# Optimization experiments

Measured on AMD Instinct MI355X. Metric: run time of the kernel, lower is better.

The kernel has to match this reference:

```python
import jax, jax.numpy as jnp
import numpy as np

B, M, N, E = 64, 100, 6400, 102400   # graphs, nodes/graph, total nodes, edges
H, D, EMB, IMG, NC = 4, 512, 768, 1024, 2
HD = H * D
EPS = 1e-5


def _bn2(x, g, b, m, v):
    # BatchNorm1d eval mode on [B, C]
    return (x - m) / jnp.sqrt(v + EPS) * g + b


def _bn3(x, g, b, m, v):
    # BatchNorm1d eval mode on [B, C, L] -> channel dim is axis 1 (node index)
    return (x - m[None, :, None]) / jnp.sqrt(v + EPS)[None, :, None] * g[None, :, None] + b[None, :, None]


def _gat(feat, src, dst, W, al, ar, bias):
    # DGL GATConv (eval: feat_drop is identity). feat: [N, F_in]
    h = (feat @ W.T).reshape(-1, H, D)                 # [N, H, D]
    el = (h * al[None]).sum(-1)                         # [N, H]
    er = (h * ar[None]).sum(-1)                         # [N, H]
    e = jax.nn.leaky_relu(el[src] + er[dst], negative_slope=0.2)  # [E, H]
    mx = jax.ops.segment_max(e, dst, num_segments=N)
    a = jnp.exp(e - mx[dst])
    s = jax.ops.segment_sum(a, dst, num_segments=N)
    alpha = a / s[dst]                                  # edge softmax over incoming edges
    out = jax.ops.segment_sum(h[src] * alpha[:, :, None], dst, num_segments=N)  # [N, H, D]
    return out + bias.reshape(1, H, D)


def setup_inputs() -> dict:
    key = jax.random.key(0)
    ks = iter(jax.random.split(key, 80))
    n = lambda *s: jax.random.normal(next(ks), s, dtype=jnp.float32)

    def bn(c):
        return (1.0 + 0.1 * n(c), 0.1 * n(c), 0.1 * n(c),
                0.5 + jax.random.uniform(next(ks), (c,), dtype=jnp.float32))

    s = 0.02
    inp = {}
    inp['img_embedding'] = n(B, IMG)
    inp['func_text_embedding'] = n(B, EMB)
    inp['unix_emb'] = n(N, EMB)
    inp['pos_emb'] = jax.random.uniform(next(ks), (N, 4), dtype=jnp.float32)
    inp['src'] = jax.random.randint(next(ks), (E,), 0, N)
    inp['dst'] = jax.random.randint(next(ks), (E,), 0, N)
    inp['gat1_W'] = n(HD, EMB) * s; inp['gat1_al'] = n(H, D) * 0.1; inp['gat1_ar'] = n(H, D) * 0.1; inp['gat1_b'] = jnp.zeros(HD)
    inp['gat2_W'] = n(HD, HD) * s; inp['gat2_al'] = n(H, D) * 0.1; inp['gat2_ar'] = n(H, D) * 0.1; inp['gat2_b'] = jnp.zeros(HD)
    inp['fc_W'] = n(D, HD) * s; inp['fc_b'] = jnp.zeros(D)
    inp['hidden_W'] = n(8, D, D) * s; inp['hidden_b'] = jnp.zeros((8, D))
    inp['bn_text_g'], inp['bn_text_b'], inp['bn_text_m'], inp['bn_text_v'] = bn(EMB)
    inp['fc_text_W'] = n(D, EMB) * s; inp['fc_text_b'] = jnp.zeros(D)
    inp['swin_g'], inp['swin_b'], inp['swin_m'], inp['swin_v'] = bn(IMG)
    inp['swinfc_W'] = n(D, IMG) * s; inp['swinfc_b'] = jnp.zeros(D)
    inp['bngat_g'], inp['bngat_b'], inp['bngat_m'], inp['bngat_v'] = bn(M)
    inp['fc_gat_W'] = n(480, D) * s; inp['fc_gat_b'] = jnp.zeros(480)
    inp['bnbb_g'], inp['bnbb_b'], inp['bnbb_m'], inp['bnbb_v'] = bn(M)
    inp['fc_bbox_W'] = n(32, 4) * s; inp['fc_bbox_b'] = jnp.zeros(32)
    inp['fbn_g'], inp['fbn_b'], inp['fbn_m'], inp['fbn_v'] = bn(3 * D)
    inp['final_W'] = n(NC, 3 * D) * s; inp['final_b'] = jnp.zeros(NC)
    return inp


def reference(img_embedding, func_text_embedding, unix_emb, pos_emb, src, dst,
              gat1_W, gat1_al, gat1_ar, gat1_b, gat2_W, gat2_al, gat2_ar, gat2_b,
              fc_W, fc_b, hidden_W, hidden_b,
              bn_text_g, bn_text_b, bn_text_m, bn_text_v, fc_text_W, fc_text_b,
              swin_g, swin_b, swin_m, swin_v, swinfc_W, swinfc_b,
              bngat_g, bngat_b, bngat_m, bngat_v, fc_gat_W, fc_gat_b,
              bnbb_g, bnbb_b, bnbb_m, bnbb_v, fc_bbox_W, fc_bbox_b,
              fbn_g, fbn_b, fbn_m, fbn_v, final_W, final_b):
    # image branch
    x = jax.nn.elu(_bn2(img_embedding, swin_g, swin_b, swin_m, swin_v) @ swinfc_W.T + swinfc_b)
    # text branch
    ft = jax.nn.elu(_bn2(func_text_embedding, bn_text_g, bn_text_b, bn_text_m, bn_text_v) @ fc_text_W.T + fc_text_b)
    # graph branch: two stacked GATConv layers (dropout is identity in eval)
    h = _gat(unix_emb, src, dst, gat1_W, gat1_al, gat1_ar, gat1_b).reshape(N, HD)
    h = _gat(h, src, dst, gat2_W, gat2_al, gat2_ar, gat2_b).reshape(N, HD)
    h = jax.nn.elu(h @ fc_W.T + fc_b)
    for i in range(8):
        h = jax.nn.elu(h @ hidden_W[i].T + hidden_b[i])
    # unbatch + pad to max_node=100 -> pure reshape (all graphs have exactly M nodes)
    h_i = h.reshape(B, M, D)
    pos_i = pos_emb.reshape(B, M, 4)
    h_i = jax.nn.elu(_bn3(h_i, bngat_g, bngat_b, bngat_m, bngat_v) @ fc_gat_W.T + fc_gat_b)      # [B, M, 480]
    pos_i = jax.nn.elu(_bn3(pos_i, bnbb_g, bnbb_b, bnbb_m, bnbb_v) @ fc_bbox_W.T + fc_bbox_b)    # [B, M, 32]
    h_feature = jnp.concatenate([h_i, pos_i], axis=2).mean(axis=1)                                # [B, 512]
    all_feats = jnp.concatenate([x, h_feature, ft], axis=1)                                       # [B, 1536]
    return _bn2(all_feats, fbn_g, fbn_b, fbn_m, fbn_v) @ final_W.T + final_b
```

## Files before the change

### kernel.cpp

```cpp
#include <hip/hip_runtime.h>
#include <math.h>

#define Bg   64
#define Mg   100
#define Ng   6400
#define Eg   102400
#define Hh   4
#define Dd   512
#define HDd  2048
#define EMBd 768
#define IMGd 1024
#define EPSc 1e-5f

typedef __bf16 bf16x8 __attribute__((ext_vector_type(8)));
typedef float  f32x4  __attribute__((ext_vector_type(4)));

#define SBAR __builtin_amdgcn_sched_barrier(0)
#define WBAR __builtin_amdgcn_s_barrier()

__device__ __forceinline__ float eluf(float x) { return x > 0.f ? x : expm1f(x); }

__device__ __forceinline__ unsigned short f2bf(float x) {
    unsigned int u = __builtin_bit_cast(unsigned int, x);
    u += 0x7FFFu + ((u >> 16) & 1u);
    return (unsigned short)(u >> 16);
}
__device__ __forceinline__ float bf2f(unsigned short s) {
    return __builtin_bit_cast(float, ((unsigned int)s) << 16);
}

__device__ __forceinline__ void gld16(const void* g, void* l) {
    __builtin_amdgcn_global_load_lds(
        (const __attribute__((address_space(1))) void*)g,
        (__attribute__((address_space(3))) void*)l, 16, 0, 0);
}

__global__ __launch_bounds__(256)
void gemm_bf16(const unsigned short* __restrict__ A,
               const unsigned short* __restrict__ W,
               const float* __restrict__ bias, void* __restrict__ C,
               int M, int N, int K, int act, int outbf)
{
    __shared__ __align__(16) unsigned short As[2][128 * 32];
    __shared__ __align__(16) unsigned short Bs[2][128 * 32];
    const int tid  = threadIdx.x;
    const int lane = tid & 63, wid = tid >> 6;
    const int bm = blockIdx.y * 128, bn = blockIdx.x * 128;
    const int wm = (wid >> 1) * 64, wn = (wid & 1) * 64;
    const int lrow = lane >> 2;
    const int lcol = (lane & 3) << 3;

    f32x4 acc[4][4] = {};

    const int ra = wid * 32;
    const unsigned short* gA0 = A + (size_t)(bm + ra + lrow) * K + lcol;
    const unsigned short* gA1 = A + (size_t)(bm + ra + 16 + lrow) * K + lcol;
    int rb0 = bn + ra + lrow;       if (rb0 >= N) rb0 = N - 1;
    int rb1 = bn + ra + 16 + lrow;  if (rb1 >= N) rb1 = N - 1;
    const unsigned short* gB0 = W + (size_t)rb0 * K + lcol;
    const unsigned short* gB1 = W + (size_t)rb1 * K + lcol;

    const int frow = lane & 15;
    const int quad = (lane >> 4) << 3;
    const int nt = K >> 5;

#define STAGE128(t, b)                                  \
    do {                                                \
        const int k0_ = (t) << 5;                       \
        gld16(gA0 + k0_, &As[b][ra * 32]);              \
        gld16(gA1 + k0_, &As[b][(ra + 16) * 32]);       \
        gld16(gB0 + k0_, &Bs[b][ra * 32]);              \
        gld16(gB1 + k0_, &Bs[b][(ra + 16) * 32]);       \
    } while (0)

    STAGE128(0, 0);
    if (nt > 1) STAGE128(1, 1);

    for (int t = 0; t < nt; ++t) {
        const int bi = t & 1;
        SBAR;
        if (t + 1 < nt) { asm volatile("s_waitcnt vmcnt(4)" ::: "memory"); }
        else            { asm volatile("s_waitcnt vmcnt(0)" ::: "memory"); }
        SBAR; WBAR; SBAR;

        bf16x8 af[4], bfr[4];
#pragma unroll
        for (int i = 0; i < 4; ++i)
            af[i]  = *(const bf16x8*)&As[bi][(wm + i * 16 + frow) * 32 + quad];
#pragma unroll
        for (int i = 0; i < 4; ++i)
            bfr[i] = *(const bf16x8*)&Bs[bi][(wn + i * 16 + frow) * 32 + quad];
#pragma unroll
        for (int mi = 0; mi < 4; ++mi)
#pragma unroll
            for (int ni = 0; ni < 4; ++ni)
                acc[mi][ni] = __builtin_amdgcn_mfma_f32_16x16x32_bf16(
                    af[mi], bfr[ni], acc[mi][ni], 0, 0, 0);

        SBAR;
        asm volatile("s_waitcnt lgkmcnt(0)" ::: "memory");
        SBAR; WBAR; SBAR;
        if (t + 2 < nt) STAGE128(t + 2, bi);
    }
#undef STAGE128

    const int crow0 = bm + wm + ((lane >> 4) << 2);
    const int ccol0 = bn + wn + (lane & 15);
#pragma unroll
    for (int mi = 0; mi < 4; ++mi) {
#pragma unroll
        for (int ni = 0; ni < 4; ++ni) {
            int col = ccol0 + ni * 16;
            if (col >= N) continue;
            float bv = bias ? bias[col] : 0.f;
#pragma unroll
            for (int r = 0; r < 4; ++r) {
                int row = crow0 + mi * 16 + r;
                float v = acc[mi][ni][r] + bv;
                if (act) v = eluf(v);
                if (outbf) ((unsigned short*)C)[(size_t)row * N + col] = f2bf(v);
                else       ((float*)C)[(size_t)row * N + col] = v;
            }
        }
    }
}

__global__ __launch_bounds__(256)
void gemm_bf16_t64(const unsigned short* __restrict__ A,
                   const unsigned short* __restrict__ W,
                   const float* __restrict__ bias, void* __restrict__ C,
                   int M, int N, int K, int act, int outbf)
{
    __shared__ __align__(16) unsigned short As[2][64 * 32];
    __shared__ __align__(16) unsigned short Bs[2][64 * 32];
    const int tid  = threadIdx.x;
    const int lane = tid & 63, wid = tid >> 6;
    const int bm = blockIdx.y * 64, bn = blockIdx.x * 64;
    const int wm = (wid >> 1) * 32, wn = (wid & 1) * 32;
    const int lrow = lane >> 2;
    const int lcol = (lane & 3) << 3;

    f32x4 acc[2][2] = {};

    const int ra = wid * 16;
    const unsigned short* gA = A + (size_t)(bm + ra + lrow) * K + lcol;
    int rb = bn + ra + lrow; if (rb >= N) rb = N - 1;
    const unsigned short* gB = W + (size_t)rb * K + lcol;

    const int frow = lane & 15;
    const int quad = (lane >> 4) << 3;
    const int nt = K >> 5;

#define STAGE64(t, b)                           \
    do {                                        \
        const int k0_ = (t) << 5;               \
        gld16(gA + k0_, &As[b][ra * 32]);       \
        gld16(gB + k0_, &Bs[b][ra * 32]);       \
    } while (0)

    STAGE64(0, 0);
    if (nt > 1) STAGE64(1, 1);

    for (int t = 0; t < nt; ++t) {
        const int bi = t & 1;
        SBAR;
        if (t + 1 < nt) { asm volatile("s_waitcnt vmcnt(2)" ::: "memory"); }
        else            { asm volatile("s_waitcnt vmcnt(0)" ::: "memory"); }
        SBAR; WBAR; SBAR;

        bf16x8 af0 = *(const bf16x8*)&As[bi][(wm + frow) * 32 + quad];
        bf16x8 af1 = *(const bf16x8*)&As[bi][(wm + 16 + frow) * 32 + quad];
        bf16x8 bf0 = *(const bf16x8*)&Bs[bi][(wn + frow) * 32 + quad];
        bf16x8 bf1 = *(const bf16x8*)&Bs[bi][(wn + 16 + frow) * 32 + quad];
        acc[0][0] = __builtin_amdgcn_mfma_f32_16x16x32_bf16(af0, bf0, acc[0][0], 0, 0, 0);
        acc[0][1] = __builtin_amdgcn_mfma_f32_16x16x32_bf16(af0, bf1, acc[0][1], 0, 0, 0);
        acc[1][0] = __builtin_amdgcn_mfma_f32_16x16x32_bf16(af1, bf0, acc[1][0], 0, 0, 0);
        acc[1][1] = __builtin_amdgcn_mfma_f32_16x16x32_bf16(af1, bf1, acc[1][1], 0, 0, 0);

        SBAR;
        asm volatile("s_waitcnt lgkmcnt(0)" ::: "memory");
        SBAR; WBAR; SBAR;
        if (t + 2 < nt) STAGE64(t + 2, bi);
    }
#undef STAGE64

    const int crow0 = bm + wm + ((lane >> 4) << 2);
    const int ccol0 = bn + wn + (lane & 15);
#pragma unroll
    for (int mi = 0; mi < 2; ++mi) {
#pragma unroll
        for (int ni = 0; ni < 2; ++ni) {
            int col = ccol0 + ni * 16;
            if (col >= N) continue;
            float bv = bias ? bias[col] : 0.f;
#pragma unroll
            for (int r = 0; r < 4; ++r) {
                int row = crow0 + mi * 16 + r;
                float v = acc[mi][ni][r] + bv;
                if (act) v = eluf(v);
                if (outbf) ((unsigned short*)C)[(size_t)row * N + col] = f2bf(v);
                else       ((float*)C)[(size_t)row * N + col] = v;
            }
        }
    }
}

__global__ __launch_bounds__(256)
void gemm_nt(const float* __restrict__ A, const float* __restrict__ W,
             const float* __restrict__ bias, float* __restrict__ C,
             int M, int N, int K, int act)
{
    __shared__ float As[16 * 68];
    __shared__ float Ws[16 * 68];
    const int tid = threadIdx.x;
    const int tx = tid & 15, ty = tid >> 4;
    const int bm = blockIdx.y * 64, bn = blockIdx.x * 64;
    const int lrow = tid >> 2;
    const int lk4  = (tid & 3) << 2;
    const int arow = bm + lrow;
    const int wrow = bn + lrow;
    const float* Aptr = A + (size_t)arow * K + lk4;
    const float* Wptr = W + (size_t)wrow * K + lk4;
    float acc[4][4] = {{0.f,0.f,0.f,0.f},{0.f,0.f,0.f,0.f},{0.f,0.f,0.f,0.f},{0.f,0.f,0.f,0.f}};

    for (int k0 = 0; k0 < K; k0 += 16) {
        float4 av = make_float4(0.f,0.f,0.f,0.f);
        float4 wv = make_float4(0.f,0.f,0.f,0.f);
        if (arow < M) av = *(const float4*)(Aptr + k0);
        if (wrow < N) wv = *(const float4*)(Wptr + k0);
        As[(lk4+0)*68 + lrow] = av.x;
        As[(lk4+1)*68 + lrow] = av.y;
        As[(lk4+2)*68 + lrow] = av.z;
        As[(lk4+3)*68 + lrow] = av.w;
        Ws[(lk4+0)*68 + lrow] = wv.x;
        Ws[(lk4+1)*68 + lrow] = wv.y;
        Ws[(lk4+2)*68 + lrow] = wv.z;
        Ws[(lk4+3)*68 + lrow] = wv.w;
        __syncthreads();
#pragma unroll
        for (int kk = 0; kk < 16; ++kk) {
            float4 a = *(const float4*)&As[kk*68 + (ty<<2)];
            float4 w = *(const float4*)&Ws[kk*68 + (tx<<2)];
            acc[0][0] += a.x*w.x; acc[0][1] += a.x*w.y; acc[0][2] += a.x*w.z; acc[0][3] += a.x*w.w;
            acc[1][0] += a.y*w.x; acc[1][1] += a.y*w.y; acc[1][2] += a.y*w.z; acc[1][3] += a.y*w.w;
            acc[2][0] += a.z*w.x; acc[2][1] += a.z*w.y; acc[2][2] += a.z*w.z; acc[2][3] += a.z*w.w;
            acc[3][0] += a.w*w.x; acc[3][1] += a.w*w.y; acc[3][2] += a.w*w.z; acc[3][3] += a.w*w.w;
        }
        __syncthreads();
    }

#pragma unroll
    for (int i = 0; i < 4; ++i) {
        int row = bm + (ty<<2) + i;
        int col = bn + (tx<<2);
        if (row < M && col < N) {
            float4 v;
            v.x = acc[i][0]; v.y = acc[i][1]; v.z = acc[i][2]; v.w = acc[i][3];
            if (bias) { v.x += bias[col]; v.y += bias[col+1]; v.z += bias[col+2]; v.w += bias[col+3]; }
            if (act == 1) { v.x = eluf(v.x); v.y = eluf(v.y); v.z = eluf(v.z); v.w = eluf(v.w); }
            *(float4*)(C + (size_t)row * N + col) = v;
        }
    }
}

struct CvtPack {
    const float* s[6];
    unsigned short* d[6];
    int n4[6];
};

__global__ void cvt_all(CvtPack p, int total4)
{
    int i = blockIdx.x * 256 + threadIdx.x;
    if (i >= total4) return;
#pragma unroll
    for (int k = 0; k < 6; ++k) {
        if (i < p.n4[k]) {
            float4 v = ((const float4*)p.s[k])[i];
            ushort4 o;
            o.x = f2bf(v.x); o.y = f2bf(v.y); o.z = f2bf(v.z); o.w = f2bf(v.w);
            ((ushort4*)p.d[k])[i] = o;
            return;
        }
        i -= p.n4[k];
    }
}

__global__ void bn_col(const float* __restrict__ x, const float* __restrict__ g,
                       const float* __restrict__ b, const float* __restrict__ m,
                       const float* __restrict__ v, float* __restrict__ y,
                       int rows, int cols)
{
    int i = blockIdx.x * 256 + threadIdx.x;
    if (i >= rows * cols) return;
    int c = i % cols;
    float inv = rsqrtf(v[c] + EPSc);
    y[i] = (x[i] - m[c]) * inv * g[c] + b[c];
}

__global__ void bn_node_b4(const ushort4* __restrict__ x, const float* __restrict__ g,
                           const float* __restrict__ b, const float* __restrict__ m,
                           const float* __restrict__ v, ushort4* __restrict__ y,
                           int total4, int Cdim4)
{
    int i = blockIdx.x * 256 + threadIdx.x;
    if (i >= total4) return;
    int n = i / Cdim4;
    int p = n % Mg;
    float sc = rsqrtf(v[p] + EPSc) * g[p];
    float sh = b[p] - m[p] * sc;
    ushort4 xv = x[i];
    ushort4 o;
    o.x = f2bf(bf2f(xv.x) * sc + sh);
    o.y = f2bf(bf2f(xv.y) * sc + sh);
    o.z = f2bf(bf2f(xv.z) * sc + sh);
    o.w = f2bf(bf2f(xv.w) * sc + sh);
    y[i] = o;
}

__global__ void zero_i32(int* __restrict__ p, int n)
{
    int i = blockIdx.x * 256 + threadIdx.x;
    if (i < n) p[i] = 0;
}

__global__ void count_dst(const int* __restrict__ dst, int* __restrict__ counts, int E)
{
    int i = blockIdx.x * 256 + threadIdx.x;
    if (i < E) atomicAdd(&counts[dst[i]], 1);
}

__global__ __launch_bounds__(1024)
void scan_excl(const int* __restrict__ counts, int* __restrict__ offs,
               int* __restrict__ cursor, int n)
{
    __shared__ int sm[1024];
    __shared__ int carry;
    if (threadIdx.x == 0) carry = 0;
    __syncthreads();
    for (int base = 0; base < n; base += 1024) {
        int i = base + (int)threadIdx.x;
        int v = (i < n) ? counts[i] : 0;
        sm[threadIdx.x] = v;
        __syncthreads();
        for (int o = 1; o < 1024; o <<= 1) {
            int t = (threadIdx.x >= (unsigned)o) ? sm[threadIdx.x - o] : 0;
            __syncthreads();
            sm[threadIdx.x] += t;
            __syncthreads();
        }
        int incl = sm[threadIdx.x];
        int myc = carry;
        if (i < n) {
            int ex = myc + incl - v;
            offs[i] = ex;
            cursor[i] = ex;
        }
        __syncthreads();
        if (threadIdx.x == 1023) carry = myc + sm[1023];
        __syncthreads();
    }
    if (threadIdx.x == 0) offs[n] = carry;
}

__global__ void scatter_edges(const int* __restrict__ dst, int* __restrict__ cursor,
                              int* __restrict__ eid, int E)
{
    int i = blockIdx.x * 256 + threadIdx.x;
    if (i < E) {
        int p = atomicAdd(&cursor[dst[i]], 1);
        eid[p] = i;
    }
}

__global__ __launch_bounds__(256)
void elr_kernel(const unsigned short* __restrict__ Hm, const float* __restrict__ al,
                const float* __restrict__ ar, float* __restrict__ el,
                float* __restrict__ er)
{
    int wid = threadIdx.x >> 6, lane = threadIdx.x & 63;
    int g = (blockIdx.x << 2) + wid;
    int n = g >> 2, h = g & 3;
    const unsigned short* hp = Hm + ((size_t)n << 11) + (h << 9) + (lane << 3);
    const float* alp = al + (h << 9) + (lane << 3);
    const float* arp = ar + (h << 9) + (lane << 3);
    ushort4 x0 = *(const ushort4*)hp;
    ushort4 x1 = *(const ushort4*)(hp + 4);
    float4 l0 = *(const float4*)alp, l1 = *(const float4*)(alp + 4);
    float4 r0 = *(const float4*)arp, r1 = *(const float4*)(arp + 4);
    float a0 = bf2f(x0.x), a1 = bf2f(x0.y), a2 = bf2f(x0.z), a3 = bf2f(x0.w);
    float a4 = bf2f(x1.x), a5 = bf2f(x1.y), a6 = bf2f(x1.z), a7 = bf2f(x1.w);
    float se = a0*l0.x + a1*l0.y + a2*l0.z + a3*l0.w + a4*l1.x + a5*l1.y + a6*l1.z + a7*l1.w;
    float sr = a0*r0.x + a1*r0.y + a2*r0.z + a3*r0.w + a4*r1.x + a5*r1.y + a6*r1.z + a7*r1.w;
#pragma unroll
    for (int o = 32; o > 0; o >>= 1) {
        se += __shfl_down(se, o, 64);
        sr += __shfl_down(sr, o, 64);
    }
    if (lane == 0) { el[g] = se; er[g] = sr; }
}

__global__ __launch_bounds__(256)
void gat_agg(const unsigned short* __restrict__ Hm, const float* __restrict__ el,
             const float* __restrict__ er, const int* __restrict__ src,
             const int* __restrict__ offs, const int* __restrict__ eid,
             const float* __restrict__ bias, unsigned short* __restrict__ out)
{
    int n = blockIdx.x;
    int tid = threadIdx.x;
    int beg = offs[n], end = offs[n + 1];
    int deg = end - beg;
    const int b0 = tid << 2;
    const int b1 = 1024 + (tid << 2);
    const int h0 = tid >> 7;
    const int h1 = h0 + 2;

    if (deg == 0) {
#pragma unroll
        for (int j = 0; j < 4; ++j) {
            out[((size_t)n << 11) + b0 + j] = f2bf(bias[b0 + j]);
            out[((size_t)n << 11) + b1 + j] = f2bf(bias[b1 + j]);
        }
        return;
    }

    __shared__ float m_sh[4], s_sh[4], al_sh[4];
    __shared__ int   src_sh[128];
    __shared__ float logit_sh[512];
    __shared__ float w_sh[512];

    if (tid < 4) { m_sh[tid] = -INFINITY; s_sh[tid] = 0.f; }
    float acc[8] = {0.f,0.f,0.f,0.f,0.f,0.f,0.f,0.f};
    __syncthreads();

    for (int c0 = 0; c0 < deg; c0 += 128) {
        int cnt = min(128, deg - c0);
        for (int i = tid; i < cnt; i += 256) src_sh[i] = src[eid[beg + c0 + i]];
        __syncthreads();
        for (int idx = tid; idx < (cnt << 2); idx += 256) {
            int i = idx >> 2, h = idx & 3;
            float x = el[(src_sh[i] << 2) + h] + er[(n << 2) + h];
            logit_sh[idx] = x > 0.f ? x : 0.2f * x;
        }
        __syncthreads();
        if (tid < 4) {
            float cm = -INFINITY;
            for (int i = 0; i < cnt; ++i) cm = fmaxf(cm, logit_sh[(i << 2) + tid]);
            float mn = fmaxf(m_sh[tid], cm);
            al_sh[tid] = expf(m_sh[tid] - mn);
            m_sh[tid] = mn;
        }
        __syncthreads();
        for (int idx = tid; idx < (cnt << 2); idx += 256)
            w_sh[idx] = expf(logit_sh[idx] - m_sh[idx & 3]);
        __syncthreads();
        if (tid < 4) {
            float cs = 0.f;
            for (int i = 0; i < cnt; ++i) cs += w_sh[(i << 2) + tid];
            s_sh[tid] = s_sh[tid] * al_sh[tid] + cs;
        }
        float r0 = al_sh[h0], r1 = al_sh[h1];
        acc[0] *= r0; acc[1] *= r0; acc[2] *= r0; acc[3] *= r0;
        acc[4] *= r1; acc[5] *= r1; acc[6] *= r1; acc[7] *= r1;
        for (int i = 0; i < cnt; ++i) {
            const unsigned short* hp = Hm + ((size_t)src_sh[i] << 11);
            ushort4 a = *(const ushort4*)(hp + b0);
            ushort4 b = *(const ushort4*)(hp + b1);
            float w0 = w_sh[(i << 2) + h0], w1 = w_sh[(i << 2) + h1];
            acc[0] += w0 * bf2f(a.x); acc[1] += w0 * bf2f(a.y);
            acc[2] += w0 * bf2f(a.z); acc[3] += w0 * bf2f(a.w);
            acc[4] += w1 * bf2f(b.x); acc[5] += w1 * bf2f(b.y);
            acc[6] += w1 * bf2f(b.z); acc[7] += w1 * bf2f(b.w);
        }
        __syncthreads();
    }

    float is0 = 1.f / s_sh[h0], is1 = 1.f / s_sh[h1];
#pragma unroll
    for (int j = 0; j < 4; ++j) {
        out[((size_t)n << 11) + b0 + j] = f2bf(acc[j] * is0 + bias[b0 + j]);
        out[((size_t)n << 11) + b1 + j] = f2bf(acc[4 + j] * is1 + bias[b1 + j]);
    }
}

__global__ void mean_kernel(const float* __restrict__ hg, const float* __restrict__ pos,
                            const float* __restrict__ bg, const float* __restrict__ bb_,
                            const float* __restrict__ bm_, const float* __restrict__ bv_,
                            const float* __restrict__ W, const float* __restrict__ bias,
                            float* __restrict__ hf)
{
    int i = blockIdx.x * 256 + threadIdx.x;
    if (i >= Bg * Dd) return;
    int bb = i >> 9, c = i & 511;
    float s = 0.f;
    if (c < 480) {
        const float* p = hg + (size_t)bb * Mg * 480 + c;
        for (int mm = 0; mm < Mg; ++mm) s += p[mm * 480];
    } else {
        int o = c - 480;
        float w0 = W[(o << 2) + 0], w1 = W[(o << 2) + 1];
        float w2 = W[(o << 2) + 2], w3 = W[(o << 2) + 3];
        float bo = bias[o];
        const float* pp = pos + (size_t)bb * Mg * 4;
        for (int mm = 0; mm < Mg; ++mm) {
            float sc = rsqrtf(bv_[mm] + EPSc) * bg[mm];
            float sh = bb_[mm] - bm_[mm] * sc;
            float a = bo + (pp[mm*4+0]*sc+sh)*w0 + (pp[mm*4+1]*sc+sh)*w1
                         + (pp[mm*4+2]*sc+sh)*w2 + (pp[mm*4+3]*sc+sh)*w3;
            s += eluf(a);
        }
    }
    hf[i] = s * 0.01f;
}

__global__ __launch_bounds__(256)
void final_kernel(const float* __restrict__ x, const float* __restrict__ hf,
                  const float* __restrict__ ft, const float* __restrict__ g,
                  const float* __restrict__ b, const float* __restrict__ m,
                  const float* __restrict__ v, const float* __restrict__ W,
                  const float* __restrict__ bias, float* __restrict__ out)
{
    int bb = blockIdx.x;
    int tid = threadIdx.x;
    float a0 = 0.f, a1 = 0.f;
    for (int c = tid; c < 1536; c += 256) {
        float xv = (c < 512) ? x[bb * 512 + c]
                 : (c < 1024) ? hf[bb * 512 + (c - 512)]
                              : ft[bb * 512 + (c - 1024)];
        float z = (xv - m[c]) * rsqrtf(v[c] + EPSc) * g[c] + b[c];
        a0 += z * W[c];
        a1 += z * W[1536 + c];
    }
    __shared__ float r0[256], r1[256];
    r0[tid] = a0; r1[tid] = a1;
    __syncthreads();
    for (int o = 128; o > 0; o >>= 1) {
        if (tid < o) { r0[tid] += r0[tid + o]; r1[tid] += r1[tid + o]; }
        __syncthreads();
    }
    if (tid == 0) {
        out[bb * 2 + 0] = r0[0] + bias[0];
        out[bb * 2 + 1] = r1[0] + bias[1];
    }
}

extern "C" void kernel_launch(void* const* d_in, const int* in_sizes, int n_in,
                              void* d_out, int out_size, void* d_ws, size_t ws_size,
                              hipStream_t stream)
{
    (void)in_sizes; (void)n_in; (void)out_size; (void)ws_size;

    const float* img   = (const float*)d_in[0];
    const float* ftxt  = (const float*)d_in[1];
    const float* unixe = (const float*)d_in[2];
    const float* pos   = (const float*)d_in[3];
    const int*   src   = (const int*)  d_in[4];
    const int*   dst   = (const int*)  d_in[5];
    const float* g1W   = (const float*)d_in[6];
    const float* g1al  = (const float*)d_in[7];
    const float* g1ar  = (const float*)d_in[8];
    const float* g1b   = (const float*)d_in[9];
    const float* g2W   = (const float*)d_in[10];
    const float* g2al  = (const float*)d_in[11];
    const float* g2ar  = (const float*)d_in[12];
    const float* g2b   = (const float*)d_in[13];
    const float* fcW   = (const float*)d_in[14];
    const float* fcb   = (const float*)d_in[15];
    const float* hidW  = (const float*)d_in[16];
    const float* hidb  = (const float*)d_in[17];
    const float* btg   = (const float*)d_in[18];
    const float* btb   = (const float*)d_in[19];
    const float* btm   = (const float*)d_in[20];
    const float* btv   = (const float*)d_in[21];
    const float* ftW   = (const float*)d_in[22];
    const float* ftbi  = (const float*)d_in[23];
    const float* swg   = (const float*)d_in[24];
    const float* swb   = (const float*)d_in[25];
    const float* swm   = (const float*)d_in[26];
    const float* swv   = (const float*)d_in[27];
    const float* swW   = (const float*)d_in[28];
    const float* swbi  = (const float*)d_in[29];
    const float* bgg   = (const float*)d_in[30];
    const float* bgb   = (const float*)d_in[31];
    const float* bgm   = (const float*)d_in[32];
    const float* bgv   = (const float*)d_in[33];
    const float* fgW   = (const float*)d_in[34];
    const float* fgb   = (const float*)d_in[35];
    const float* bbgp  = (const float*)d_in[36];
    const float* bbbp  = (const float*)d_in[37];
    const float* bbmp  = (const float*)d_in[38];
    const float* bbvp  = (const float*)d_in[39];
    const float* fbW   = (const float*)d_in[40];
    const float* fbb   = (const float*)d_in[41];
    const float* fng   = (const float*)d_in[42];
    const float* fnb   = (const float*)d_in[43];
    const float* fnm   = (const float*)d_in[44];
    const float* fnv   = (const float*)d_in[45];
    const float* fiW   = (const float*)d_in[46];
    const float* fib   = (const float*)d_in[47];
    float* out = (float*)d_out;

    char* p = (char*)d_ws;
    unsigned short* fA  = (unsigned short*)p; p += (size_t)Ng * HDd * 2;
    unsigned short* fB  = (unsigned short*)p; p += (size_t)Ng * HDd * 2;
    unsigned short* fC  = (unsigned short*)p; p += (size_t)Ng * Dd * 2;
    unsigned short* fD  = (unsigned short*)p; p += (size_t)Ng * Dd * 2;
    float*          fE  = (float*)p;          p += (size_t)Ng * 480 * 4;
    float*          el  = (float*)p;          p += (size_t)Ng * Hh * 4;
    float*          er  = (float*)p;          p += (size_t)Ng * Hh * 4;
    float*          xb  = (float*)p;          p += (size_t)Bg * Dd * 4;
    float*          ftb = (float*)p;          p += (size_t)Bg * Dd * 4;
    float*          hf  = (float*)p;          p += (size_t)Bg * Dd * 4;
    float*          ti  = (float*)p;          p += (size_t)Bg * IMGd * 4;
    float*          tt  = (float*)p;          p += (size_t)Bg * EMBd * 4;
    unsigned short* ubf = (unsigned short*)p; p += (size_t)Ng * EMBd * 2;
    unsigned short* wg1 = (unsigned short*)p; p += (size_t)HDd * EMBd * 2;
    unsigned short* wg2 = (unsigned short*)p; p += (size_t)HDd * HDd * 2;
    unsigned short* wfc = (unsigned short*)p; p += (size_t)Dd * HDd * 2;
    unsigned short* whid= (unsigned short*)p; p += (size_t)8 * Dd * Dd * 2;
    unsigned short* wfg = (unsigned short*)p; p += (size_t)480 * Dd * 2;
    int* counts = (int*)p; p += (size_t)Ng * 4;
    int* offs   = (int*)p; p += (size_t)(Ng + 1) * 4 + 12;
    int* cursor = (int*)p; p += (size_t)Ng * 4;
    int* eid    = (int*)p; p += (size_t)Eg * 4;

    CvtPack cp;
    cp.s[0] = unixe; cp.d[0] = ubf;  cp.n4[0] = Ng * EMBd / 4;
    cp.s[1] = g1W;   cp.d[1] = wg1;  cp.n4[1] = HDd * EMBd / 4;
    cp.s[2] = g2W;   cp.d[2] = wg2;  cp.n4[2] = HDd * HDd / 4;
    cp.s[3] = fcW;   cp.d[3] = wfc;  cp.n4[3] = Dd * HDd / 4;
    cp.s[4] = hidW;  cp.d[4] = whid; cp.n4[4] = 8 * Dd * Dd / 4;
    cp.s[5] = fgW;   cp.d[5] = wfg;  cp.n4[5] = 480 * Dd / 4;
    int total4 = cp.n4[0] + cp.n4[1] + cp.n4[2] + cp.n4[3] + cp.n4[4] + cp.n4[5];
    cvt_all<<<(total4 + 255)/256, 256, 0, stream>>>(cp, total4);

    bn_col<<<(Bg*IMGd + 255)/256, 256, 0, stream>>>(img, swg, swb, swm, swv, ti, Bg, IMGd);
    gemm_nt<<<dim3(8, 1), 256, 0, stream>>>(ti, swW, swbi, xb, Bg, Dd, IMGd, 1);
    bn_col<<<(Bg*EMBd + 255)/256, 256, 0, stream>>>(ftxt, btg, btb, btm, btv, tt, Bg, EMBd);
    gemm_nt<<<dim3(8, 1), 256, 0, stream>>>(tt, ftW, ftbi, ftb, Bg, Dd, EMBd, 1);

    zero_i32<<<(Ng + 255)/256, 256, 0, stream>>>(counts, Ng);
    count_dst<<<(Eg + 255)/256, 256, 0, stream>>>(dst, counts, Eg);
    scan_excl<<<1, 1024, 0, stream>>>(counts, offs, cursor, Ng);
    scatter_edges<<<(Eg + 255)/256, 256, 0, stream>>>(dst, cursor, eid, Eg);

    gemm_bf16<<<dim3(HDd/128, Ng/128), 256, 0, stream>>>(ubf, wg1, nullptr, fA, Ng, HDd, EMBd, 0, 1);
    elr_kernel<<<Ng, 256, 0, stream>>>(fA, g1al, g1ar, el, er);
    gat_agg<<<Ng, 256, 0, stream>>>(fA, el, er, src, offs, eid, g1b, fB);

    gemm_bf16<<<dim3(HDd/128, Ng/128), 256, 0, stream>>>(fB, wg2, nullptr, fA, Ng, HDd, HDd, 0, 1);
    elr_kernel<<<Ng, 256, 0, stream>>>(fA, g2al, g2ar, el, er);
    gat_agg<<<Ng, 256, 0, stream>>>(fA, el, er, src, offs, eid, g2b, fB);

    gemm_bf16_t64<<<dim3(Dd/64, Ng/64), 256, 0, stream>>>(fB, wfc, fcb, fC, Ng, Dd, HDd, 1, 1);

    unsigned short* cur = fC; unsigned short* nxt = fD;
    for (int i = 0; i < 8; ++i) {
        gemm_bf16_t64<<<dim3(Dd/64, Ng/64), 256, 0, stream>>>(
            cur, whid + (size_t)i * Dd * Dd, hidb + (size_t)i * Dd, nxt, Ng, Dd, Dd, 1, 1);
        unsigned short* t = cur; cur = nxt; nxt = t;
    }

    bn_node_b4<<<(Ng*Dd/4 + 255)/256, 256, 0, stream>>>(
        (const ushort4*)cur, bgg, bgb, bgm, bgv, (ushort4*)nxt, Ng*Dd/4, Dd/4);
    gemm_bf16_t64<<<dim3(8, Ng/64), 256, 0, stream>>>(nxt, wfg, fgb, fE, Ng, 480, Dd, 1, 0);

    mean_kernel<<<(Bg*Dd + 255)/256, 256, 0, stream>>>(fE, pos, bbgp, bbbp, bbmp, bbvp, fbW, fbb, hf);

    final_kernel<<<Bg, 256, 0, stream>>>(xb, hf, ftb, fng, fnb, fnm, fnv, fiW, fib, out);
}
```

Measured before the change: 818.9 us.

## Replace GAT projection GEMM with 256x256-tile, 8-wave pipelined swizzled kernel

Adds a new bf16 GEMM for the two GAT projections that uses 256x256 output tiles, 512 threads, a K-step of 64, XOR-swizzled LDS layout and a finely interleaved load/MFMA schedule with setprio hints. The aim is more data reuse per block and less LDS bank conflict and stall time. The trade-off is a far smaller grid (200 blocks for 256 CUs), 128 KB of LDS per block, and the loss of the N bounds check.

```diff
diff --git a/kernel.cpp b/kernel.cpp
--- a/kernel.cpp
+++ b/kernel.cpp
@@ -17,6 +17,7 @@
 
 #define SBAR __builtin_amdgcn_sched_barrier(0)
 #define WBAR __builtin_amdgcn_s_barrier()
+#define BARRIER do { SBAR; WBAR; SBAR; } while (0)
 
 __device__ __forceinline__ float eluf(float x) { return x > 0.f ? x : expm1f(x); }
 
@@ -35,88 +36,144 @@
         (__attribute__((address_space(3))) void*)l, 16, 0, 0);
 }
 
-__global__ __launch_bounds__(256)
-void gemm_bf16(const unsigned short* __restrict__ A,
-               const unsigned short* __restrict__ W,
-               const float* __restrict__ bias, void* __restrict__ C,
-               int M, int N, int K, int act, int outbf)
-{
-    __shared__ __align__(16) unsigned short As[2][128 * 32];
-    __shared__ __align__(16) unsigned short Bs[2][128 * 32];
+__global__ __launch_bounds__(512, 2)
+void gemm_bf16_256(const unsigned short* __restrict__ A,
+                   const unsigned short* __restrict__ W,
+                   const float* __restrict__ bias, void* __restrict__ C,
+                   int M, int N, int K, int act, int outbf)
+{
+    __shared__ __align__(16) unsigned short As[2][256 * 64];
+    __shared__ __align__(16) unsigned short Bs[2][256 * 64];
+
     const int tid  = threadIdx.x;
     const int lane = tid & 63, wid = tid >> 6;
-    const int bm = blockIdx.y * 128, bn = blockIdx.x * 128;
-    const int wm = (wid >> 1) * 64, wn = (wid & 1) * 64;
-    const int lrow = lane >> 2;
-    const int lcol = (lane & 3) << 3;
-
-    f32x4 acc[4][4] = {};
-
-    const int ra = wid * 32;
-    const unsigned short* gA0 = A + (size_t)(bm + ra + lrow) * K + lcol;
-    const unsigned short* gA1 = A + (size_t)(bm + ra + 16 + lrow) * K + lcol;
-    int rb0 = bn + ra + lrow;       if (rb0 >= N) rb0 = N - 1;
-    int rb1 = bn + ra + 16 + lrow;  if (rb1 >= N) rb1 = N - 1;
-    const unsigned short* gB0 = W + (size_t)rb0 * K + lcol;
-    const unsigned short* gB1 = W + (size_t)rb1 * K + lcol;
-
-    const int frow = lane & 15;
-    const int quad = (lane >> 4) << 3;
-    const int nt = K >> 5;
-
-#define STAGE128(t, b)                                  \
-    do {                                                \
-        const int k0_ = (t) << 5;                       \
-        gld16(gA0 + k0_, &As[b][ra * 32]);              \
-        gld16(gA1 + k0_, &As[b][(ra + 16) * 32]);       \
-        gld16(gB0 + k0_, &Bs[b][ra * 32]);              \
-        gld16(gB1 + k0_, &Bs[b][(ra + 16) * 32]);       \
+    const int wm = wid >> 2, wn = wid & 3;
+    const int bm = blockIdx.y * 256, bn = blockIdx.x * 256;
+    const int fl = lane & 15;
+    const int kb = (lane >> 4) << 4;
+    const int sx = ((lane >> 2) & 1) << 5;
+
+    f32x4 acc[8][4] = {};
+    bf16x8 a_[4][2];
+    bf16x8 b_[2][2][2];
+
+    const int NT = K >> 6;
+
+    const int srow0 = tid >> 3;
+    const int scol  = (((tid & 7) ^ (((tid >> 5) & 1) << 1)) << 3);
+    const unsigned short* pAs = A + (size_t)(bm + srow0) * K + scol;
+    const unsigned short* pBs = W + (size_t)(bn + srow0) * K + scol;
+    const size_t K64 = (size_t)K * 64, K128 = (size_t)K * 128;
+
+#define STGA(kt, h, d)                                                        \
+    do {                                                                      \
+        gld16(pAs + (h) * K128 + ((kt) << 6),                                 \
+              (char*)As[d] + (h) * 16384 + wid * 1024);                       \
+        gld16(pAs + (h) * K128 + K64 + ((kt) << 6),                           \
+              (char*)As[d] + (h) * 16384 + 8192 + wid * 1024);                \
     } while (0)
-
-    STAGE128(0, 0);
-    if (nt > 1) STAGE128(1, 1);
-
-    for (int t = 0; t < nt; ++t) {
-        const int bi = t & 1;
+#define STGB(kt, h, d)                                                        \
+    do {                                                                      \
+        gld16(pBs + (h) * K128 + ((kt) << 6),                                 \
+              (char*)Bs[d] + (h) * 16384 + wid * 1024);                       \
+        gld16(pBs + (h) * K128 + K64 + ((kt) << 6),                           \
+              (char*)Bs[d] + (h) * 16384 + 8192 + wid * 1024);                \
+    } while (0)
+
+#define LDA(qm, d)                                                            \
+    _Pragma("unroll") for (int i = 0; i < 4; ++i)                             \
+    _Pragma("unroll") for (int kk = 0; kk < 2; ++kk) {                        \
+        int r_  = wm * 128 + (qm) * 64 + i * 16 + fl;                         \
+        int pb_ = r_ * 128 + ((kk * 64 + kb) ^ sx);                           \
+        a_[i][kk] = *(const bf16x8*)((const char*)As[d] + pb_);               \
+    }
+#define LDB(qn, d)                                                            \
+    _Pragma("unroll") for (int j = 0; j < 2; ++j)                             \
+    _Pragma("unroll") for (int kk = 0; kk < 2; ++kk) {                        \
+        int r_  = wn * 64 + (qn) * 32 + j * 16 + fl;                          \
+        int pb_ = r_ * 128 + ((kk * 64 + kb) ^ sx);                           \
+        b_[qn][j][kk] = *(const bf16x8*)((const char*)Bs[d] + pb_);           \
+    }
+#define MM(qm, qn)                                                            \
+    do {                                                                      \
+        __builtin_amdgcn_s_setprio(1);                                        \
+        _Pragma("unroll") for (int kk = 0; kk < 2; ++kk)                      \
+        _Pragma("unroll") for (int i = 0; i < 4; ++i)                         \
+        _Pragma("unroll") for (int j = 0; j < 2; ++j)                         \
+            acc[(qm) * 4 + i][(qn) * 2 + j] =                                 \
+                __builtin_amdgcn_mfma_f32_16x16x32_bf16(                      \
+                    a_[i][kk], b_[qn][j][kk],                                 \
+                    acc[(qm) * 4 + i][(qn) * 2 + j], 0, 0, 0);                \
+        __builtin_amdgcn_s_setprio(0);                                        \
+    } while (0)
+
+    STGB(0, 0, 0); STGB(0, 1, 0);
+    STGA(0, 0, 0); STGA(0, 1, 0);
+    STGB(1, 0, 1); STGB(1, 1, 1);
+    SBAR; asm volatile("s_waitcnt vmcnt(4)" ::: "memory"); SBAR;
+    BARRIER;
+
+    for (int j = 0; j < (NT >> 1); ++j) {
+        const int O = 2 * j + 1;
+        const int g1 = (2 * j + 2 < NT), g2 = (2 * j + 3 < NT);
+
+        LDA(0, 0); LDB(0, 0);
+        STGA(O, 0, 1);
+        BARRIER; MM(0, 0); BARRIER;
+
+        LDB(1, 0);
+        STGA(O, 1, 1);
+        BARRIER; MM(0, 1); BARRIER;
+
+        LDA(1, 0);
+        if (g1) STGB(2 * j + 2, 0, 0);
+        BARRIER; MM(1, 0); BARRIER;
+
+        if (g1) STGB(2 * j + 2, 1, 0);
         SBAR;
-        if (t + 1 < nt) { asm volatile("s_waitcnt vmcnt(4)" ::: "memory"); }
-        else            { asm volatile("s_waitcnt vmcnt(0)" ::: "memory"); }
-        SBAR; WBAR; SBAR;
-
-        bf16x8 af[4], bfr[4];
-#pragma unroll
-        for (int i = 0; i < 4; ++i)
-            af[i]  = *(const bf16x8*)&As[bi][(wm + i * 16 + frow) * 32 + quad];
-#pragma unroll
-        for (int i = 0; i < 4; ++i)
-            bfr[i] = *(const bf16x8*)&Bs[bi][(wn + i * 16 + frow) * 32 + quad];
-#pragma unroll
-        for (int mi = 0; mi < 4; ++mi)
-#pragma unroll
-            for (int ni = 0; ni < 4; ++ni)
-                acc[mi][ni] = __builtin_amdgcn_mfma_f32_16x16x32_bf16(
-                    af[mi], bfr[ni], acc[mi][ni], 0, 0, 0);
-
+        if (g1) { asm volatile("s_waitcnt vmcnt(4)" ::: "memory"); }
+        else    { asm volatile("s_waitcnt vmcnt(0)" ::: "memory"); }
         SBAR;
-        asm volatile("s_waitcnt lgkmcnt(0)" ::: "memory");
-        SBAR; WBAR; SBAR;
-        if (t + 2 < nt) STAGE128(t + 2, bi);
-    }
-#undef STAGE128
-
-    const int crow0 = bm + wm + ((lane >> 4) << 2);
-    const int ccol0 = bn + wn + (lane & 15);
-#pragma unroll
-    for (int mi = 0; mi < 4; ++mi) {
-#pragma unroll
-        for (int ni = 0; ni < 4; ++ni) {
-            int col = ccol0 + ni * 16;
-            if (col >= N) continue;
+        BARRIER; MM(1, 1); BARRIER;
+
+        LDA(0, 1); LDB(0, 1);
+        if (g1) STGA(2 * j + 2, 0, 0);
+        BARRIER; MM(0, 0); BARRIER;
+
+        LDB(1, 1);
+        if (g1) STGA(2 * j + 2, 1, 0);
+        BARRIER; MM(0, 1); BARRIER;
+
+        LDA(1, 1);
+        if (g2) STGB(2 * j + 3, 0, 1);
+        BARRIER; MM(1, 0); BARRIER;
+
+        if (g2) STGB(2 * j + 3, 1, 1);
+        SBAR;
+        if (g1) { asm volatile("s_waitcnt vmcnt(4)" ::: "memory"); }
+        else    { asm volatile("s_waitcnt vmcnt(0)" ::: "memory"); }
+        SBAR;
+        BARRIER; MM(1, 1); BARRIER;
+    }
+
+#undef STGA
+#undef STGB
+#undef LDA
+#undef LDB
+#undef MM
+
+    const int crow0 = bm + wm * 128 + ((lane >> 4) << 2);
+    const int ccol0 = bn + wn * 64 + fl;
+#pragma unroll
+    for (int fr = 0; fr < 8; ++fr) {
+#pragma unroll
+        for (int fc = 0; fc < 4; ++fc) {
+            int col = ccol0 + fc * 16;
             float bv = bias ? bias[col] : 0.f;
 #pragma unroll
-            for (int r = 0; r < 4; ++r) {
-                int row = crow0 + mi * 16 + r;
-                float v = acc[mi][ni][r] + bv;
+            for (int rr = 0; rr < 4; ++rr) {
+                int row = crow0 + fr * 16 + rr;
+                float v = acc[fr][fc][rr] + bv;
                 if (act) v = eluf(v);
                 if (outbf) ((unsigned short*)C)[(size_t)row * N + col] = f2bf(v);
                 else       ((float*)C)[(size_t)row * N + col] = v;
@@ -644,11 +701,11 @@
     scan_excl<<<1, 1024, 0, stream>>>(counts, offs, cursor, Ng);
     scatter_edges<<<(Eg + 255)/256, 256, 0, stream>>>(dst, cursor, eid, Eg);
 
-    gemm_bf16<<<dim3(HDd/128, Ng/128), 256, 0, stream>>>(ubf, wg1, nullptr, fA, Ng, HDd, EMBd, 0, 1);
+    gemm_bf16_256<<<dim3(HDd/256, Ng/256), 512, 0, stream>>>(ubf, wg1, nullptr, fA, Ng, HDd, EMBd, 0, 1);
     elr_kernel<<<Ng, 256, 0, stream>>>(fA, g1al, g1ar, el, er);
     gat_agg<<<Ng, 256, 0, stream>>>(fA, el, er, src, offs, eid, g1b, fB);
 
-    gemm_bf16<<<dim3(HDd/128, Ng/128), 256, 0, stream>>>(fB, wg2, nullptr, fA, Ng, HDd, HDd, 0, 1);
+    gemm_bf16_256<<<dim3(HDd/256, Ng/256), 512, 0, stream>>>(fB, wg2, nullptr, fA, Ng, HDd, HDd, 0, 1);
     elr_kernel<<<Ng, 256, 0, stream>>>(fA, g2al, g2ar, el, er);
     gat_agg<<<Ng, 256, 0, stream>>>(fA, el, er, src, offs, eid, g2b, fB);
 
```

After: 799.0 us. -2.4%, faster.
